# Kernel optimization log

Measured on AMD Instinct MI355X. Metric: run time of the kernel, lower is better.

## Reference

```python
import jax, jax.numpy as jnp
import numpy as np

N = 50000      # nodes
E = 640000     # edges
DIN = 128      # input feature dim
DOUT = 128     # env net output dim
DACT = 2       # action net output dim (keep/drop logits)
REL = 100      # relation embedding dim (hard-coded in get_net)
T = 2          # num edge types
TAU = 0.5      # gumbel temperature (CoGNN temp)


def _lin(k, i, o):
    return jax.random.normal(k, (o, i), jnp.float32) * np.float32(1.0 / np.sqrt(i))


def _hgn_params(key, din, dout):
    ks = jax.random.split(key, 5)
    return {"W_w": _lin(ks[0], din, dout), "W_b": jnp.zeros((dout,), jnp.float32),
            "Wr_w": _lin(ks[1], REL, dout), "Wr_b": jnp.zeros((dout,), jnp.float32),
            "a_w": _lin(ks[2], 3 * dout, 1), "a_b": jnp.zeros((1,), jnp.float32),
            "Wres_w": _lin(ks[3], din, dout), "Wres_b": jnp.zeros((dout,), jnp.float32),
            "rel_emb": jax.random.normal(ks[4], (T, REL), jnp.float32)}


def setup_inputs():
    key = jax.random.key(0)
    ks = jax.random.split(key, 8)
    inp = {"x": jax.random.normal(ks[0], (N, DIN), jnp.float32),
           "edge_index": jax.random.randint(ks[1], (2, E), 0, N, jnp.int32),
           "edge_type": jax.random.randint(ks[2], (E,), 0, T, jnp.int32)}
    u_in = jax.random.uniform(ks[3], (N, DACT), jnp.float32, 1e-6, 1.0 - 1e-6)
    u_out = jax.random.uniform(ks[4], (N, DACT), jnp.float32, 1e-6, 1.0 - 1e-6)
    inp["g_in"] = -jnp.log(-jnp.log(u_in))    # Gumbel(0,1) noise
    inp["g_out"] = -jnp.log(-jnp.log(u_out))
    for name, k, dout in (("inA", ks[5], DACT), ("outA", ks[6], DACT), ("env", ks[7], DOUT)):
        for pk, pv in _hgn_params(k, DIN, dout).items():
            inp[name + "_" + pk] = pv
    return inp


def _simple_hgn(x, src, dst, etype, W_w, W_b, Wr_w, Wr_b, a_w, a_b, Wres_w, Wres_b, rel_emb, mask=None):
    # out = scatter_add_dst( alpha_e * W x_src ) + W_res x   (SimpleHGN, add aggr)
    n = x.shape[0]
    dout = W_w.shape[0]
    h = x @ W_w.T + W_b                       # [N, dout] = W(x)
    r = rel_emb @ Wr_w.T + Wr_b               # [T, dout] = W_r(rel_emb)
    # a(cat(W(x_i), W(x_j), W_r(rel))) decomposed into three per-node/per-type dot products
    a1, a2, a3 = a_w[0, :dout], a_w[0, dout:2 * dout], a_w[0, 2 * dout:]
    s_dst = h @ a1                            # [N]
    s_src = h @ a2                            # [N]
    s_rel = r @ a3                            # [T]
    logits = jax.nn.leaky_relu(s_dst[dst] + s_src[src] + s_rel[etype] + a_b[0], 0.2)  # [E]
    if mask is not None:
        logits = jnp.where(mask, logits, -1e9)
    m = jax.ops.segment_max(logits, dst, num_segments=n)
    e = jnp.exp(logits - m[dst])
    if mask is not None:
        e = jnp.where(mask, e, 0.0)
    denom = jax.ops.segment_sum(e, dst, num_segments=n)
    alpha = e / jnp.maximum(denom[dst], 1e-16)   # edge softmax over incoming edges of each target
    aggr = jax.ops.segment_sum(h[src] * alpha[:, None], dst, num_segments=n)
    return aggr + x @ Wres_w.T + Wres_b


def _gumbel_hard(logits, g):
    y = jax.nn.softmax((logits + g) / TAU, axis=-1)
    y_hard = jax.nn.one_hot(jnp.argmax(y, axis=-1), y.shape[-1], dtype=y.dtype)
    return y_hard + y - jax.lax.stop_gradient(y)   # straight-through (hard=True)


def reference(x, edge_index, edge_type, g_in, g_out,
              inA_W_w, inA_W_b, inA_Wr_w, inA_Wr_b, inA_a_w, inA_a_b, inA_Wres_w, inA_Wres_b, inA_rel_emb,
              outA_W_w, outA_W_b, outA_Wr_w, outA_Wr_b, outA_a_w, outA_a_b, outA_Wres_w, outA_Wres_b, outA_rel_emb,
              env_W_w, env_W_b, env_Wr_w, env_Wr_b, env_a_w, env_a_b, env_Wres_w, env_Wres_b, env_rel_emb):
    src, dst = edge_index[0], edge_index[1]
    in_logits = _simple_hgn(x, src, dst, edge_type, inA_W_w, inA_W_b, inA_Wr_w, inA_Wr_b,
                            inA_a_w, inA_a_b, inA_Wres_w, inA_Wres_b, inA_rel_emb)
    out_logits = _simple_hgn(x, src, dst, edge_type, outA_W_w, outA_W_b, outA_Wr_w, outA_Wr_b,
                             outA_a_w, outA_a_b, outA_Wres_w, outA_Wres_b, outA_rel_emb)
    in_p = _gumbel_hard(in_logits, g_in)
    out_p = _gumbel_hard(out_logits, g_out)
    edge_weight = in_p[:, 0][dst] * out_p[:, 0][src]   # keep_in[v] * keep_out[u]
    mask = edge_weight > 0                              # hard edge filtering, non-differentiable as in torch
    return _simple_hgn(x, src, dst, edge_type, env_W_w, env_W_b, env_Wr_w, env_Wr_b,
                       env_a_w, env_a_b, env_Wres_w, env_Wres_b, env_rel_emb, mask=mask)
```

## Files before the change

### kernel.cpp

```cpp
#include <hip/hip_runtime.h>
#include <hip/hip_bf16.h>
#include <hip/hip_fp16.h>
#include <cstddef>

#define N_NODES 50000
#define N_EDGES 640000
#define DEG_CAP 48

__device__ __forceinline__ float lrelu(float z) { return z >= 0.f ? z : 0.2f * z; }

__device__ __forceinline__ unsigned short f2bf(float f) {
    unsigned u = __builtin_bit_cast(unsigned, f);
    u += 0x7FFFu + ((u >> 16) & 1u);
    return (unsigned short)(u >> 16);
}
__device__ __forceinline__ float bf2f(unsigned short h) {
    unsigned u = ((unsigned)h) << 16;
    return __builtin_bit_cast(float, u);
}

typedef __attribute__((ext_vector_type(8))) short short8;
typedef __attribute__((ext_vector_type(4))) float floatx4;

__global__ __launch_bounds__(256) void k_setup(
    const float* __restrict__ x,
    const float* __restrict__ rel_in, const float* __restrict__ Wr_in,
    const float* __restrict__ Wrb_in,
    const float* __restrict__ rel_out, const float* __restrict__ Wr_out,
    const float* __restrict__ Wrb_out,
    const float* __restrict__ rel_env, const float* __restrict__ Wr_env,
    const float* __restrict__ Wrb_env,
    const float* __restrict__ Wi, const float* __restrict__ Wib,
    const float* __restrict__ WiR, const float* __restrict__ WiRb,
    const float* __restrict__ ai,
    const float* __restrict__ Wo, const float* __restrict__ Wob,
    const float* __restrict__ WoR, const float* __restrict__ WoRb,
    const float* __restrict__ ao,
    const float* __restrict__ eW, const float* __restrict__ eWb,
    const float* __restrict__ eWR, const float* __restrict__ ea,
    float* __restrict__ srel,
    unsigned short* __restrict__ wh, unsigned short* __restrict__ wl,
    float4* __restrict__ dstT, float4* __restrict__ srcPack,
    float4* __restrict__ res_pack)
{
    int b = blockIdx.x;
    int tid = threadIdx.x;

    if (b == 0) {
        __shared__ float red[256];
        __shared__ float rs[8];
        {
            int tt = tid >> 7, j = tid & 127;
            float acc = 0.f;
            for (int k = 0; k < 100; ++k) acc += rel_env[tt * 100 + k] * Wr_env[j * 100 + k];
            acc += Wrb_env[j];
            red[tid] = acc * ea[256 + j];
        }
        if (tid < 8) {
            int net = tid >> 2, tt = (tid >> 1) & 1, j = tid & 1;
            const float* re = net ? rel_out : rel_in;
            const float* wr = net ? Wr_out : Wr_in;
            const float* wb = net ? Wrb_out : Wrb_in;
            float acc = 0.f;
            for (int k = 0; k < 100; ++k) acc += re[tt * 100 + k] * wr[j * 100 + k];
            rs[tid] = acc + wb[j];
        }
        __syncthreads();
        if (tid < 2) {
            float s = 0.f;
            for (int j = 0; j < 128; ++j) s += red[tid * 128 + j];
            srel[4 + tid] = s;
        } else if (tid == 2) {
            srel[0] = rs[0] * ai[4] + rs[1] * ai[5];
            srel[1] = rs[2] * ai[4] + rs[3] * ai[5];
        } else if (tid == 3) {
            srel[2] = rs[4] * ao[4] + rs[5] * ao[5];
            srel[3] = rs[6] * ao[4] + rs[7] * ao[5];
        }
        return;
    }
    if (b < 129) {
        int i = (b - 1) * 256 + tid;
        float v = (i < 16384) ? eW[i] : eWR[i - 16384];
        unsigned short h = f2bf(v);
        wh[i] = h;
        wl[i] = f2bf(v - bf2f(h));
        return;
    }

    __shared__ float sw[10][128];
    __shared__ float vb[2];
    {
        int row = tid >> 5, c4 = tid & 31;
        const float* src;
        switch (row) {
            case 0: src = Wi;        break;
            case 1: src = Wi + 128;  break;
            case 2: src = WiR;       break;
            case 3: src = WiR + 128; break;
            case 4: src = Wo;        break;
            case 5: src = Wo + 128;  break;
            case 6: src = WoR;       break;
            default: src = WoR + 128; break;
        }
        float4 v = ((const float4*)src)[c4];
        sw[row][c4 * 4 + 0] = v.x; sw[row][c4 * 4 + 1] = v.y;
        sw[row][c4 * 4 + 2] = v.z; sw[row][c4 * 4 + 3] = v.w;
    }
    {
        int half = tid >> 7, k = tid & 127;
        const float* av = ea + half * 128;
        float s = 0.f;
        for (int j = 0; j < 128; ++j) s += eW[j * 128 + k] * av[j];
        sw[8 + half][k] = s;
    }
    if (tid < 2) {
        const float* av2 = ea + tid * 128;
        float sb = 0.f;
        for (int j = 0; j < 128; ++j) sb += eWb[j] * av2[j];
        vb[tid] = sb;
    }
    __syncthreads();
    int n = (b - 129) * 256 + tid;
    if (n >= N_NODES) return;
    const float4* xr = (const float4*)(x + (size_t)n * 128);
    float a0 = 0, a1 = 0, a2 = 0, a3 = 0, a4 = 0, a5 = 0, a6 = 0, a7 = 0;
    float a8 = 0, a9 = 0;
#pragma unroll 8
    for (int k4 = 0; k4 < 32; ++k4) {
        float4 v = xr[k4];
        int k = k4 * 4;
        a0 += v.x * sw[0][k] + v.y * sw[0][k + 1] + v.z * sw[0][k + 2] + v.w * sw[0][k + 3];
        a1 += v.x * sw[1][k] + v.y * sw[1][k + 1] + v.z * sw[1][k + 2] + v.w * sw[1][k + 3];
        a2 += v.x * sw[2][k] + v.y * sw[2][k + 1] + v.z * sw[2][k + 2] + v.w * sw[2][k + 3];
        a3 += v.x * sw[3][k] + v.y * sw[3][k + 1] + v.z * sw[3][k + 2] + v.w * sw[3][k + 3];
        a4 += v.x * sw[4][k] + v.y * sw[4][k + 1] + v.z * sw[4][k + 2] + v.w * sw[4][k + 3];
        a5 += v.x * sw[5][k] + v.y * sw[5][k + 1] + v.z * sw[5][k + 2] + v.w * sw[5][k + 3];
        a6 += v.x * sw[6][k] + v.y * sw[6][k + 1] + v.z * sw[6][k + 2] + v.w * sw[6][k + 3];
        a7 += v.x * sw[7][k] + v.y * sw[7][k + 1] + v.z * sw[7][k + 2] + v.w * sw[7][k + 3];
        a8 += v.x * sw[8][k] + v.y * sw[8][k + 1] + v.z * sw[8][k + 2] + v.w * sw[8][k + 3];
        a9 += v.x * sw[9][k] + v.y * sw[9][k + 1] + v.z * sw[9][k + 2] + v.w * sw[9][k + 3];
    }
    float hi0 = a0 + Wib[0], hi1 = a1 + Wib[1];
    float ri0 = a2 + WiRb[0], ri1 = a3 + WiRb[1];
    float ho0 = a4 + Wob[0], ho1 = a5 + Wob[1];
    float ro0 = a6 + WoRb[0], ro1 = a7 + WoRb[1];
    float sdi = hi0 * ai[0] + hi1 * ai[1];
    float ssi = hi0 * ai[2] + hi1 * ai[3];
    float sdo = ho0 * ao[0] + ho1 * ao[1];
    float sso = ho0 * ao[2] + ho1 * ao[3];
    dstT[n]           = make_float4(sdi, sdo, a8 + vb[0], 0.f);
    srcPack[2 * n]     = make_float4(ssi, sso, a9 + vb[1], 0.f);
    srcPack[2 * n + 1] = make_float4(hi0, hi1, ho0, ho1);
    res_pack[n]       = make_float4(ri0, ri1, ro0, ro1);
}

__global__ __launch_bounds__(256) void k_scatter(
    const int* __restrict__ ei, const int* __restrict__ et,
    const float4* __restrict__ dstT, const float4* __restrict__ srcPack,
    const float* __restrict__ srel, const float* __restrict__ ab_env,
    int* __restrict__ cursor, unsigned long long* __restrict__ recs)
{
    int e = blockIdx.x * 256 + threadIdx.x;
    if (e >= N_EDGES) return;
    int src = ei[e], dst = ei[N_EDGES + e], t = et[e];
    float s4 = srel[4], s5 = srel[5];
    float abe = ab_env[0];
    float4 dT = dstT[dst];
    float4 sT = srcPack[2 * src];
    float le = lrelu(dT.z + sT.z + (t ? s5 : s4) + abe);
    int pos = atomicAdd(&cursor[dst], 1);
    if (pos < DEG_CAP) {
        unsigned lo = (unsigned)(src | (t << 20));
        unsigned hi = (unsigned)__float_as_int(__expf(le));
        unsigned long long rec = ((unsigned long long)hi << 32) | lo;
        __builtin_nontemporal_store(rec, &recs[dst * DEG_CAP + pos]);
    }
}

__global__ __launch_bounds__(256) void k_action_seg(
    const int* __restrict__ cursor, const unsigned long long* __restrict__ recs,
    const float4* __restrict__ dstT, const float4* __restrict__ srcPack,
    const float4* __restrict__ res_pack,
    const float* __restrict__ srel,
    const float* __restrict__ ab_in, const float* __restrict__ ab_out,
    const float* __restrict__ g_in, const float* __restrict__ g_out,
    unsigned char* __restrict__ flags)
{
    int gid = blockIdx.x * 256 + threadIdx.x;
    int n = gid >> 2, sub = gid & 3;
    if (n >= N_NODES) return;
    int cnt = min(cursor[n], DEG_CAP);
    int st = n * DEG_CAP;
    float s0 = srel[0], s1 = srel[1], s2 = srel[2], s3 = srel[3];
    float abi = ab_in[0], abo = ab_out[0];
    float4 dT = dstT[n];
    float ni0 = 0, ni1 = 0, di = 0, no0 = 0, no1 = 0, dob = 0;
    for (int i = sub; i < cnt; i += 4) {
        unsigned long long rec = recs[st + i];
        int src = (int)(rec & 0xFFFFFu);
        int t = (int)((rec >> 20) & 0xFFFu);
        float4 sT = srcPack[2 * src];
        float4 hp = srcPack[2 * src + 1];
        float li = lrelu(dT.x + sT.x + (t ? s1 : s0) + abi);
        float lo = lrelu(dT.y + sT.y + (t ? s3 : s2) + abo);
        float ein = __expf(li), eout = __expf(lo);
        di  += ein;  ni0 += ein * hp.x;  ni1 += ein * hp.y;
        dob += eout; no0 += eout * hp.z; no1 += eout * hp.w;
    }
#pragma unroll
    for (int o = 1; o < 4; o <<= 1) {
        ni0 += __shfl_down(ni0, o); ni1 += __shfl_down(ni1, o);
        di  += __shfl_down(di,  o);
        no0 += __shfl_down(no0, o); no1 += __shfl_down(no1, o);
        dob += __shfl_down(dob, o);
    }
    if (sub == 0) {
        float4 rp = res_pack[n];
        float dinv = 1.f / fmaxf(di, 1e-16f);
        float l0 = ni0 * dinv + rp.x;
        float l1 = ni1 * dinv + rp.y;
        float2 gi = ((const float2*)g_in)[n];
        int in0 = (l0 + gi.x) >= (l1 + gi.y);
        float oinv = 1.f / fmaxf(dob, 1e-16f);
        float m0 = no0 * oinv + rp.z;
        float m1 = no1 * oinv + rp.w;
        float2 go = ((const float2*)g_out)[n];
        int out0 = (m0 + go.x) >= (m1 + go.y);
        flags[n] = (unsigned char)(in0 | (out0 << 1));
    }
}

__global__ __launch_bounds__(256, 2) void k_env_mfma(
    const float* __restrict__ x,
    const unsigned short* __restrict__ wh, const unsigned short* __restrict__ wl,
    const float* __restrict__ Wb, const float* __restrict__ WRb,
    __half* __restrict__ h_env, float* __restrict__ dout)
{
    int tid = threadIdx.x;
    int lane = tid & 63;
    int wv = tid >> 6;
    int l15 = lane & 15;
    int quad = lane >> 4;
    int jbase = wv * 64;

    short8 bh[4][4], bl[4][4];
    float bias[4];
#pragma unroll
    for (int jtl = 0; jtl < 4; ++jtl) {
        int j = jbase + jtl * 16 + l15;
        bias[jtl] = (j < 128) ? Wb[j] : WRb[j - 128];
#pragma unroll
        for (int ks = 0; ks < 4; ++ks) {
            size_t o = (size_t)j * 128 + ks * 32 + quad * 8;
            bh[jtl][ks] = *(const short8*)(wh + o);
            bl[jtl][ks] = *(const short8*)(wl + o);
        }
    }

    for (int t = blockIdx.x; t < 3125; t += gridDim.x) {
        int node = t * 16 + l15;
        const float4* ap = (const float4*)(x + (size_t)node * 128 + quad * 8);
        float4 f[8];
#pragma unroll
        for (int ks = 0; ks < 4; ++ks) {
            f[2 * ks]     = ap[ks * 8];
            f[2 * ks + 1] = ap[ks * 8 + 1];
        }
        short8 ah[4], al[4];
#pragma unroll
        for (int ks = 0; ks < 4; ++ks) {
            float av[8] = {f[2 * ks].x, f[2 * ks].y, f[2 * ks].z, f[2 * ks].w,
                           f[2 * ks + 1].x, f[2 * ks + 1].y, f[2 * ks + 1].z, f[2 * ks + 1].w};
#pragma unroll
            for (int i = 0; i < 8; ++i) {
                unsigned short h = f2bf(av[i]);
                ah[ks][i] = (short)h;
                al[ks][i] = (short)f2bf(av[i] - bf2f(h));
            }
        }
        floatx4 acc[4];
#pragma unroll
        for (int jtl = 0; jtl < 4; ++jtl) acc[jtl] = (floatx4)(0.f);
#pragma unroll
        for (int ks = 0; ks < 4; ++ks) {
#pragma unroll
            for (int jtl = 0; jtl < 4; ++jtl) {
                acc[jtl] = __builtin_amdgcn_mfma_f32_16x16x32_bf16(ah[ks], bh[jtl][ks], acc[jtl], 0, 0, 0);
                acc[jtl] = __builtin_amdgcn_mfma_f32_16x16x32_bf16(al[ks], bh[jtl][ks], acc[jtl], 0, 0, 0);
                acc[jtl] = __builtin_amdgcn_mfma_f32_16x16x32_bf16(ah[ks], bl[jtl][ks], acc[jtl], 0, 0, 0);
            }
        }
        int nb = t * 16 + quad * 4;
        if (wv < 2) {
#pragma unroll
            for (int jtl = 0; jtl < 4; ++jtl) {
                int j = jbase + jtl * 16 + l15;
#pragma unroll
                for (int r = 0; r < 4; ++r)
                    h_env[(size_t)(nb + r) * 128 + j] = __float2half(acc[jtl][r] + bias[jtl]);
            }
        } else {
#pragma unroll
            for (int jtl = 0; jtl < 4; ++jtl) {
                int j = jbase - 128 + jtl * 16 + l15;
#pragma unroll
                for (int r = 0; r < 4; ++r)
                    dout[(size_t)(nb + r) * 128 + j] = acc[jtl][r] + bias[jtl];
            }
        }
    }
}

__global__ __launch_bounds__(256) void k_aggr(
    const int* __restrict__ cursor,
    const unsigned long long* __restrict__ recs, const unsigned char* __restrict__ flags,
    const __half* __restrict__ h_env, float* __restrict__ dout)
{
    __shared__ int   s_src[4][64];
    __shared__ float s_w[4][64];
    int tid = threadIdx.x;
    int lane = tid & 63;
    int wv = tid >> 6;
    int n = blockIdx.x * 4 + wv;
    if (n >= N_NODES) return;
    if (!(flags[n] & 1)) return;
    int cnt = min(cursor[n], DEG_CAP);
    int st = n * DEG_CAP;
    float ax = 0.f, ay = 0.f, den = 0.f;
    const __half2* h2 = (const __half2*)h_env;
    {
        int i = lane;
        bool act = false; int src = 0; float wgt = 0.f;
        if (i < cnt) {
            unsigned long long rec = recs[st + i];
            src = (int)(rec & 0xFFFFFu);
            wgt = __int_as_float((int)(rec >> 32));
            act = (flags[src] & 2) != 0;
        }
        unsigned long long bal = __ballot(act);
        int m = __popcll(bal);
        if (act) {
            int pos = __popcll(bal & ((1ull << lane) - 1));
            s_src[wv][pos] = src;
            s_w[wv][pos] = wgt;
        }
        __builtin_amdgcn_wave_barrier();
        int k = 0;
        for (; k + 4 <= m; k += 4) {
            int s0 = s_src[wv][k], s1 = s_src[wv][k + 1];
            int s2 = s_src[wv][k + 2], s3 = s_src[wv][k + 3];
            float w0 = s_w[wv][k], w1 = s_w[wv][k + 1];
            float w2 = s_w[wv][k + 2], w3 = s_w[wv][k + 3];
            float2 f0 = __half22float2(h2[(size_t)s0 * 64 + lane]);
            float2 f1 = __half22float2(h2[(size_t)s1 * 64 + lane]);
            float2 f2 = __half22float2(h2[(size_t)s2 * 64 + lane]);
            float2 f3 = __half22float2(h2[(size_t)s3 * 64 + lane]);
            den += (w0 + w1) + (w2 + w3);
            ax += w0 * f0.x + w1 * f1.x + w2 * f2.x + w3 * f3.x;
            ay += w0 * f0.y + w1 * f1.y + w2 * f2.y + w3 * f3.y;
        }
        for (; k < m; ++k) {
            int s0 = s_src[wv][k];
            float w0 = s_w[wv][k];
            float2 f0 = __half22float2(h2[(size_t)s0 * 64 + lane]);
            den += w0; ax += w0 * f0.x; ay += w0 * f0.y;
        }
    }
    float inv = 1.f / fmaxf(den, 1e-16f);
    float2* op = (float2*)dout + (size_t)n * 64 + lane;
    float2 r = *op;
    r.x = ax * inv + r.x;
    r.y = ay * inv + r.y;
    *op = r;
}

extern "C" void kernel_launch(void* const* d_in, const int* in_sizes, int n_in,
                              void* d_out, int out_size, void* d_ws, size_t ws_size,
                              hipStream_t stream)
{
    const float* x     = (const float*)d_in[0];
    const int*   ei    = (const int*)d_in[1];
    const int*   et    = (const int*)d_in[2];
    const float* g_in  = (const float*)d_in[3];
    const float* g_out = (const float*)d_in[4];
    const float* iW   = (const float*)d_in[5];
    const float* iWb  = (const float*)d_in[6];
    const float* iWr  = (const float*)d_in[7];
    const float* iWrb = (const float*)d_in[8];
    const float* ia   = (const float*)d_in[9];
    const float* iab  = (const float*)d_in[10];
    const float* iWR  = (const float*)d_in[11];
    const float* iWRb = (const float*)d_in[12];
    const float* irel = (const float*)d_in[13];
    const float* oW   = (const float*)d_in[14];
    const float* oWb  = (const float*)d_in[15];
    const float* oWr  = (const float*)d_in[16];
    const float* oWrb = (const float*)d_in[17];
    const float* oa   = (const float*)d_in[18];
    const float* oab  = (const float*)d_in[19];
    const float* oWR  = (const float*)d_in[20];
    const float* oWRb = (const float*)d_in[21];
    const float* orel = (const float*)d_in[22];
    const float* eW   = (const float*)d_in[23];
    const float* eWb  = (const float*)d_in[24];
    const float* eWr  = (const float*)d_in[25];
    const float* eWrb = (const float*)d_in[26];
    const float* ea   = (const float*)d_in[27];
    const float* eab  = (const float*)d_in[28];
    const float* eWR  = (const float*)d_in[29];
    const float* eWRb = (const float*)d_in[30];
    const float* erel = (const float*)d_in[31];
    float* dout = (float*)d_out;

    char* w = (char*)d_ws;
    size_t off = 0;
    auto alloc = [&](size_t bytes) -> char* {
        char* p = w + off;
        off += (bytes + 255) & ~(size_t)255;
        return p;
    };
    int*   cursor  = (int*)alloc((size_t)N_NODES * 4);
    size_t zeroBytes = off;
    float* srel    = (float*)alloc(16 * 4);
    float4* dstT     = (float4*)alloc((size_t)4 * N_NODES * 4);
    float4* srcPack  = (float4*)alloc((size_t)8 * N_NODES * 4);
    float4* res_pack = (float4*)alloc((size_t)4 * N_NODES * 4);
    unsigned char* flags = (unsigned char*)alloc(N_NODES);
    unsigned short* wh = (unsigned short*)alloc((size_t)32768 * 2);
    unsigned short* wl = (unsigned short*)alloc((size_t)32768 * 2);
    unsigned long long* recs = (unsigned long long*)alloc((size_t)N_NODES * DEG_CAP * 8);
    __half* h_env    = (__half*)alloc((size_t)N_NODES * 128 * 2);

    (void)hipMemsetAsync(w, 0, zeroBytes, stream);
    k_setup<<<325, 256, 0, stream>>>(x,
                                     irel, iWr, iWrb, orel, oWr, oWrb, erel, eWr, eWrb,
                                     iW, iWb, iWR, iWRb, ia, oW, oWb, oWR, oWRb, oa,
                                     eW, eWb, eWR, ea,
                                     srel, wh, wl, dstT, srcPack, res_pack);
    k_scatter<<<2500, 256, 0, stream>>>(ei, et, dstT, srcPack, srel, eab,
                                        cursor, recs);
    k_env_mfma<<<512, 256, 0, stream>>>(x, wh, wl, eWb, eWRb, h_env, dout);
    k_action_seg<<<782, 256, 0, stream>>>(cursor, recs, dstT, srcPack, res_pack,
                                          srel, iab, oab, g_in, g_out, flags);
    k_aggr<<<12500, 256, 0, stream>>>(cursor, recs, flags, h_env, dout);
}
```

Before: 246.8 us.

## Precompute action-net edge exponentials in scatter and fold cursor zeroing into setup

The scatter kernel now computes the in/out action attention exponentials per edge alongside the env weight and stores them in a 16-byte record, so the action segment kernel no longer gathers srcPack[2*src] and recomputes lrelu/exp. The separate memset of the cursor array is removed and the zeroing moves into k_setup, which saves one launch. In exchange the record buffer doubles in size, so scatter writes and the record reads in k_aggr move twice the bytes. k_aggr now reads 16-byte records even though it only needs 8 bytes of each.

```diff
diff --git a/kernel.cpp b/kernel.cpp
--- a/kernel.cpp
+++ b/kernel.cpp
@@ -21,6 +21,7 @@
 
 typedef __attribute__((ext_vector_type(8))) short short8;
 typedef __attribute__((ext_vector_type(4))) float floatx4;
+typedef __attribute__((ext_vector_type(4))) int intx4;
 
 __global__ __launch_bounds__(256) void k_setup(
     const float* __restrict__ x,
@@ -41,7 +42,7 @@
     float* __restrict__ srel,
     unsigned short* __restrict__ wh, unsigned short* __restrict__ wl,
     float4* __restrict__ dstT, float4* __restrict__ srcPack,
-    float4* __restrict__ res_pack)
+    float4* __restrict__ res_pack, int* __restrict__ cursor)
 {
     int b = blockIdx.x;
     int tid = threadIdx.x;
@@ -87,6 +88,9 @@
         wl[i] = f2bf(v - bf2f(h));
         return;
     }
+
+    int n = (b - 129) * 256 + tid;
+    if (n < N_NODES) cursor[n] = 0;
 
     __shared__ float sw[10][128];
     __shared__ float vb[2];
@@ -121,7 +125,6 @@
         vb[tid] = sb;
     }
     __syncthreads();
-    int n = (b - 129) * 256 + tid;
     if (n >= N_NODES) return;
     const float4* xr = (const float4*)(x + (size_t)n * 128);
     float a0 = 0, a1 = 0, a2 = 0, a3 = 0, a4 = 0, a5 = 0, a6 = 0, a7 = 0;
@@ -158,32 +161,36 @@
 __global__ __launch_bounds__(256) void k_scatter(
     const int* __restrict__ ei, const int* __restrict__ et,
     const float4* __restrict__ dstT, const float4* __restrict__ srcPack,
-    const float* __restrict__ srel, const float* __restrict__ ab_env,
-    int* __restrict__ cursor, unsigned long long* __restrict__ recs)
+    const float* __restrict__ srel,
+    const float* __restrict__ ab_in, const float* __restrict__ ab_out,
+    const float* __restrict__ ab_env,
+    int* __restrict__ cursor, intx4* __restrict__ recs)
 {
     int e = blockIdx.x * 256 + threadIdx.x;
     if (e >= N_EDGES) return;
     int src = ei[e], dst = ei[N_EDGES + e], t = et[e];
-    float s4 = srel[4], s5 = srel[5];
-    float abe = ab_env[0];
+    float s0 = srel[0], s1 = srel[1], s2 = srel[2];
+    float s3 = srel[3], s4 = srel[4], s5 = srel[5];
+    float abi = ab_in[0], abo = ab_out[0], abe = ab_env[0];
     float4 dT = dstT[dst];
     float4 sT = srcPack[2 * src];
+    float li = lrelu(dT.x + sT.x + (t ? s1 : s0) + abi);
+    float lo = lrelu(dT.y + sT.y + (t ? s3 : s2) + abo);
     float le = lrelu(dT.z + sT.z + (t ? s5 : s4) + abe);
     int pos = atomicAdd(&cursor[dst], 1);
     if (pos < DEG_CAP) {
-        unsigned lo = (unsigned)(src | (t << 20));
-        unsigned hi = (unsigned)__float_as_int(__expf(le));
-        unsigned long long rec = ((unsigned long long)hi << 32) | lo;
+        intx4 rec;
+        rec[0] = src | (t << 20);
+        rec[1] = __float_as_int(__expf(le));
+        rec[2] = __float_as_int(__expf(li));
+        rec[3] = __float_as_int(__expf(lo));
         __builtin_nontemporal_store(rec, &recs[dst * DEG_CAP + pos]);
     }
 }
 
 __global__ __launch_bounds__(256) void k_action_seg(
-    const int* __restrict__ cursor, const unsigned long long* __restrict__ recs,
-    const float4* __restrict__ dstT, const float4* __restrict__ srcPack,
-    const float4* __restrict__ res_pack,
-    const float* __restrict__ srel,
-    const float* __restrict__ ab_in, const float* __restrict__ ab_out,
+    const int* __restrict__ cursor, const intx4* __restrict__ recs,
+    const float4* __restrict__ srcPack, const float4* __restrict__ res_pack,
     const float* __restrict__ g_in, const float* __restrict__ g_out,
     unsigned char* __restrict__ flags)
 {
@@ -192,19 +199,12 @@
     if (n >= N_NODES) return;
     int cnt = min(cursor[n], DEG_CAP);
     int st = n * DEG_CAP;
-    float s0 = srel[0], s1 = srel[1], s2 = srel[2], s3 = srel[3];
-    float abi = ab_in[0], abo = ab_out[0];
-    float4 dT = dstT[n];
     float ni0 = 0, ni1 = 0, di = 0, no0 = 0, no1 = 0, dob = 0;
     for (int i = sub; i < cnt; i += 4) {
-        unsigned long long rec = recs[st + i];
-        int src = (int)(rec & 0xFFFFFu);
-        int t = (int)((rec >> 20) & 0xFFFu);
-        float4 sT = srcPack[2 * src];
+        intx4 r = recs[st + i];
+        int src = r[0] & 0xFFFFF;
         float4 hp = srcPack[2 * src + 1];
-        float li = lrelu(dT.x + sT.x + (t ? s1 : s0) + abi);
-        float lo = lrelu(dT.y + sT.y + (t ? s3 : s2) + abo);
-        float ein = __expf(li), eout = __expf(lo);
+        float ein = __int_as_float(r[2]), eout = __int_as_float(r[3]);
         di  += ein;  ni0 += ein * hp.x;  ni1 += ein * hp.y;
         dob += eout; no0 += eout * hp.z; no1 += eout * hp.w;
     }
@@ -314,7 +314,7 @@
 
 __global__ __launch_bounds__(256) void k_aggr(
     const int* __restrict__ cursor,
-    const unsigned long long* __restrict__ recs, const unsigned char* __restrict__ flags,
+    const intx4* __restrict__ recs, const unsigned char* __restrict__ flags,
     const __half* __restrict__ h_env, float* __restrict__ dout)
 {
     __shared__ int   s_src[4][64];
@@ -333,9 +333,9 @@
         int i = lane;
         bool act = false; int src = 0; float wgt = 0.f;
         if (i < cnt) {
-            unsigned long long rec = recs[st + i];
-            src = (int)(rec & 0xFFFFFu);
-            wgt = __int_as_float((int)(rec >> 32));
+            intx4 r = recs[st + i];
+            src = r[0] & 0xFFFFF;
+            wgt = __int_as_float(r[1]);
             act = (flags[src] & 2) != 0;
         }
         unsigned long long bal = __ballot(act);
@@ -421,7 +421,6 @@
         return p;
     };
     int*   cursor  = (int*)alloc((size_t)N_NODES * 4);
-    size_t zeroBytes = off;
     float* srel    = (float*)alloc(16 * 4);
     float4* dstT     = (float4*)alloc((size_t)4 * N_NODES * 4);
     float4* srcPack  = (float4*)alloc((size_t)8 * N_NODES * 4);
@@ -429,19 +428,18 @@
     unsigned char* flags = (unsigned char*)alloc(N_NODES);
     unsigned short* wh = (unsigned short*)alloc((size_t)32768 * 2);
     unsigned short* wl = (unsigned short*)alloc((size_t)32768 * 2);
-    unsigned long long* recs = (unsigned long long*)alloc((size_t)N_NODES * DEG_CAP * 8);
+    intx4* recs      = (intx4*)alloc((size_t)N_NODES * DEG_CAP * 16);
     __half* h_env    = (__half*)alloc((size_t)N_NODES * 128 * 2);
 
-    (void)hipMemsetAsync(w, 0, zeroBytes, stream);
     k_setup<<<325, 256, 0, stream>>>(x,
                                      irel, iWr, iWrb, orel, oWr, oWrb, erel, eWr, eWrb,
                                      iW, iWb, iWR, iWRb, ia, oW, oWb, oWR, oWRb, oa,
                                      eW, eWb, eWR, ea,
-                                     srel, wh, wl, dstT, srcPack, res_pack);
-    k_scatter<<<2500, 256, 0, stream>>>(ei, et, dstT, srcPack, srel, eab,
-                                        cursor, recs);
+                                     srel, wh, wl, dstT, srcPack, res_pack, cursor);
+    k_scatter<<<2500, 256, 0, stream>>>(ei, et, dstT, srcPack, srel,
+                                        iab, oab, eab, cursor, recs);
     k_env_mfma<<<512, 256, 0, stream>>>(x, wh, wl, eWb, eWRb, h_env, dout);
-    k_action_seg<<<782, 256, 0, stream>>>(cursor, recs, dstT, srcPack, res_pack,
-                                          srel, iab, oab, g_in, g_out, flags);
+    k_action_seg<<<782, 256, 0, stream>>>(cursor, recs, srcPack, res_pack,
+                                          g_in, g_out, flags);
     k_aggr<<<12500, 256, 0, stream>>>(cursor, recs, flags, h_env, dout);
 }
```

Measured after the change: 252.8 us. 1.02x slower.

## Fuse edge scatter and env MFMA GEMM into one kernel, drop memset

Applied to the files above, without the earlier changes.

Merges the edge-scatter kernel and the env-net MFMA GEMM into a single launch. Blocks 0-511 run the GEMM and the remaining 625 blocks each bucket 4 edges per thread, so the two independent stages can overlap on the GPU. The cursor array is now zeroed inside k_setup rather than by a separate memset, and the scatter stores become plain stores instead of nontemporal ones. This removes a launch and a memset, in exchange for mixed-role blocks that may compete for CUs and registers.

```diff
diff --git a/kernel.cpp b/kernel.cpp
--- a/kernel.cpp
+++ b/kernel.cpp
@@ -41,7 +41,7 @@
     float* __restrict__ srel,
     unsigned short* __restrict__ wh, unsigned short* __restrict__ wl,
     float4* __restrict__ dstT, float4* __restrict__ srcPack,
-    float4* __restrict__ res_pack)
+    float4* __restrict__ res_pack, int* __restrict__ cursor)
 {
     int b = blockIdx.x;
     int tid = threadIdx.x;
@@ -87,6 +87,9 @@
         wl[i] = f2bf(v - bf2f(h));
         return;
     }
+
+    int n = (b - 129) * 256 + tid;
+    if (n < N_NODES) cursor[n] = 0;
 
     __shared__ float sw[10][128];
     __shared__ float vb[2];
@@ -121,7 +124,6 @@
         vb[tid] = sb;
     }
     __syncthreads();
-    int n = (b - 129) * 256 + tid;
     if (n >= N_NODES) return;
     const float4* xr = (const float4*)(x + (size_t)n * 128);
     float a0 = 0, a1 = 0, a2 = 0, a3 = 0, a4 = 0, a5 = 0, a6 = 0, a7 = 0;
@@ -155,26 +157,121 @@
     res_pack[n]       = make_float4(ri0, ri1, ro0, ro1);
 }
 
-__global__ __launch_bounds__(256) void k_scatter(
+__global__ __launch_bounds__(256, 2) void k_mid(
+    const float* __restrict__ x,
+    const unsigned short* __restrict__ wh, const unsigned short* __restrict__ wl,
+    const float* __restrict__ Wb, const float* __restrict__ WRb,
+    __half* __restrict__ h_env, float* __restrict__ dout,
     const int* __restrict__ ei, const int* __restrict__ et,
     const float4* __restrict__ dstT, const float4* __restrict__ srcPack,
     const float* __restrict__ srel, const float* __restrict__ ab_env,
     int* __restrict__ cursor, unsigned long long* __restrict__ recs)
 {
-    int e = blockIdx.x * 256 + threadIdx.x;
-    if (e >= N_EDGES) return;
-    int src = ei[e], dst = ei[N_EDGES + e], t = et[e];
-    float s4 = srel[4], s5 = srel[5];
-    float abe = ab_env[0];
-    float4 dT = dstT[dst];
-    float4 sT = srcPack[2 * src];
-    float le = lrelu(dT.z + sT.z + (t ? s5 : s4) + abe);
-    int pos = atomicAdd(&cursor[dst], 1);
-    if (pos < DEG_CAP) {
-        unsigned lo = (unsigned)(src | (t << 20));
-        unsigned hi = (unsigned)__float_as_int(__expf(le));
-        unsigned long long rec = ((unsigned long long)hi << 32) | lo;
-        __builtin_nontemporal_store(rec, &recs[dst * DEG_CAP + pos]);
+    int b = blockIdx.x;
+    int tid = threadIdx.x;
+
+    if (b >= 512) {
+        int base = (b - 512) * 1024 + tid;
+        float s4 = srel[4], s5 = srel[5];
+        float abe = ab_env[0];
+        int src[4], dst[4], t[4];
+#pragma unroll
+        for (int k = 0; k < 4; ++k) {
+            int e = base + k * 256;
+            src[k] = ei[e];
+            dst[k] = ei[N_EDGES + e];
+            t[k]   = et[e];
+        }
+        float4 dT[4], sT[4];
+#pragma unroll
+        for (int k = 0; k < 4; ++k) {
+            dT[k] = dstT[dst[k]];
+            sT[k] = srcPack[2 * src[k]];
+        }
+#pragma unroll
+        for (int k = 0; k < 4; ++k) {
+            float le = lrelu(dT[k].z + sT[k].z + (t[k] ? s5 : s4) + abe);
+            int pos = atomicAdd(&cursor[dst[k]], 1);
+            if (pos < DEG_CAP) {
+                unsigned lo = (unsigned)(src[k] | (t[k] << 20));
+                unsigned hi = (unsigned)__float_as_int(__expf(le));
+                recs[dst[k] * DEG_CAP + pos] = ((unsigned long long)hi << 32) | lo;
+            }
+        }
+        return;
+    }
+
+    int lane = tid & 63;
+    int wv = tid >> 6;
+    int l15 = lane & 15;
+    int quad = lane >> 4;
+    int jbase = wv * 64;
+
+    short8 bh[4][4], bl[4][4];
+    float bias[4];
+#pragma unroll
+    for (int jtl = 0; jtl < 4; ++jtl) {
+        int j = jbase + jtl * 16 + l15;
+        bias[jtl] = (j < 128) ? Wb[j] : WRb[j - 128];
+#pragma unroll
+        for (int ks = 0; ks < 4; ++ks) {
+            size_t o = (size_t)j * 128 + ks * 32 + quad * 8;
+            bh[jtl][ks] = *(const short8*)(wh + o);
+            bl[jtl][ks] = *(const short8*)(wl + o);
+        }
+    }
+
+    for (int t = b; t < 3125; t += 512) {
+        int node = t * 16 + l15;
+        const float4* ap = (const float4*)(x + (size_t)node * 128 + quad * 8);
+        float4 f[8];
+#pragma unroll
+        for (int ks = 0; ks < 4; ++ks) {
+            f[2 * ks]     = ap[ks * 8];
+            f[2 * ks + 1] = ap[ks * 8 + 1];
+        }
+        short8 ah[4], al[4];
+#pragma unroll
+        for (int ks = 0; ks < 4; ++ks) {
+            float av[8] = {f[2 * ks].x, f[2 * ks].y, f[2 * ks].z, f[2 * ks].w,
+                           f[2 * ks + 1].x, f[2 * ks + 1].y, f[2 * ks + 1].z, f[2 * ks + 1].w};
+#pragma unroll
+            for (int i = 0; i < 8; ++i) {
+                unsigned short h = f2bf(av[i]);
+                ah[ks][i] = (short)h;
+                al[ks][i] = (short)f2bf(av[i] - bf2f(h));
+            }
+        }
+        floatx4 acc[4];
+#pragma unroll
+        for (int jtl = 0; jtl < 4; ++jtl) acc[jtl] = (floatx4)(0.f);
+#pragma unroll
+        for (int ks = 0; ks < 4; ++ks) {
+#pragma unroll
+            for (int jtl = 0; jtl < 4; ++jtl) {
+                acc[jtl] = __builtin_amdgcn_mfma_f32_16x16x32_bf16(ah[ks], bh[jtl][ks], acc[jtl], 0, 0, 0);
+                acc[jtl] = __builtin_amdgcn_mfma_f32_16x16x32_bf16(al[ks], bh[jtl][ks], acc[jtl], 0, 0, 0);
+                acc[jtl] = __builtin_amdgcn_mfma_f32_16x16x32_bf16(ah[ks], bl[jtl][ks], acc[jtl], 0, 0, 0);
+            }
+        }
+        int nb = t * 16 + quad * 4;
+        if (wv < 2) {
+#pragma unroll
+            for (int jtl = 0; jtl < 4; ++jtl) {
+                int j = jbase + jtl * 16 + l15;
+#pragma unroll
+                for (int r = 0; r < 4; ++r)
+                    h_env[(size_t)(nb + r) * 128 + j] = __float2half(acc[jtl][r] + bias[jtl]);
+            }
+        } else {
+#pragma unroll
+            for (int jtl = 0; jtl < 4; ++jtl) {
+                int j = jbase - 128 + jtl * 16 + l15;
+#pragma unroll
+                for (int r = 0; r < 4; ++r)
+                    dout[(size_t)(nb + r) * 128 + j] = acc[jtl][r] + bias[jtl];
+            }
+        }
     }
 }
 
@@ -228,87 +325,6 @@
         float2 go = ((const float2*)g_out)[n];
         int out0 = (m0 + go.x) >= (m1 + go.y);
         flags[n] = (unsigned char)(in0 | (out0 << 1));
-    }
-}
-
-__global__ __launch_bounds__(256, 2) void k_env_mfma(
-    const float* __restrict__ x,
-    const unsigned short* __restrict__ wh, const unsigned short* __restrict__ wl,
-    const float* __restrict__ Wb, const float* __restrict__ WRb,
-    __half* __restrict__ h_env, float* __restrict__ dout)
-{
-    int tid = threadIdx.x;
-    int lane = tid & 63;
-    int wv = tid >> 6;
-    int l15 = lane & 15;
-    int quad = lane >> 4;
-    int jbase = wv * 64;
-
-    short8 bh[4][4], bl[4][4];
-    float bias[4];
-#pragma unroll
-    for (int jtl = 0; jtl < 4; ++jtl) {
-        int j = jbase + jtl * 16 + l15;
-        bias[jtl] = (j < 128) ? Wb[j] : WRb[j - 128];
-#pragma unroll
-        for (int ks = 0; ks < 4; ++ks) {
-            size_t o = (size_t)j * 128 + ks * 32 + quad * 8;
-            bh[jtl][ks] = *(const short8*)(wh + o);
-            bl[jtl][ks] = *(const short8*)(wl + o);
-        }
-    }
-
-    for (int t = blockIdx.x; t < 3125; t += gridDim.x) {
-        int node = t * 16 + l15;
-        const float4* ap = (const float4*)(x + (size_t)node * 128 + quad * 8);
-        float4 f[8];
-#pragma unroll
-        for (int ks = 0; ks < 4; ++ks) {
-            f[2 * ks]     = ap[ks * 8];
-            f[2 * ks + 1] = ap[ks * 8 + 1];
-        }
-        short8 ah[4], al[4];
-#pragma unroll
-        for (int ks = 0; ks < 4; ++ks) {
-            float av[8] = {f[2 * ks].x, f[2 * ks].y, f[2 * ks].z, f[2 * ks].w,
-                           f[2 * ks + 1].x, f[2 * ks + 1].y, f[2 * ks + 1].z, f[2 * ks + 1].w};
-#pragma unroll
-            for (int i = 0; i < 8; ++i) {
-                unsigned short h = f2bf(av[i]);
-                ah[ks][i] = (short)h;
-                al[ks][i] = (short)f2bf(av[i] - bf2f(h));
-            }
-        }
-        floatx4 acc[4];
-#pragma unroll
-        for (int jtl = 0; jtl < 4; ++jtl) acc[jtl] = (floatx4)(0.f);
-#pragma unroll
-        for (int ks = 0; ks < 4; ++ks) {
-#pragma unroll
-            for (int jtl = 0; jtl < 4; ++jtl) {
-                acc[jtl] = __builtin_amdgcn_mfma_f32_16x16x32_bf16(ah[ks], bh[jtl][ks], acc[jtl], 0, 0, 0);
-                acc[jtl] = __builtin_amdgcn_mfma_f32_16x16x32_bf16(al[ks], bh[jtl][ks], acc[jtl], 0, 0, 0);
-                acc[jtl] = __builtin_amdgcn_mfma_f32_16x16x32_bf16(ah[ks], bl[jtl][ks], acc[jtl], 0, 0, 0);
-            }
-        }
-        int nb = t * 16 + quad * 4;
-        if (wv < 2) {
-#pragma unroll
-            for (int jtl = 0; jtl < 4; ++jtl) {
-                int j = jbase + jtl * 16 + l15;
-#pragma unroll
-                for (int r = 0; r < 4; ++r)
-                    h_env[(size_t)(nb + r) * 128 + j] = __float2half(acc[jtl][r] + bias[jtl]);
-            }
-        } else {
-#pragma unroll
-            for (int jtl = 0; jtl < 4; ++jtl) {
-                int j = jbase - 128 + jtl * 16 + l15;
-#pragma unroll
-                for (int r = 0; r < 4; ++r)
-                    dout[(size_t)(nb + r) * 128 + j] = acc[jtl][r] + bias[jtl];
-            }
-        }
     }
 }
 
@@ -421,7 +437,6 @@
         return p;
     };
     int*   cursor  = (int*)alloc((size_t)N_NODES * 4);
-    size_t zeroBytes = off;
     float* srel    = (float*)alloc(16 * 4);
     float4* dstT     = (float4*)alloc((size_t)4 * N_NODES * 4);
     float4* srcPack  = (float4*)alloc((size_t)8 * N_NODES * 4);
@@ -432,15 +447,13 @@
     unsigned long long* recs = (unsigned long long*)alloc((size_t)N_NODES * DEG_CAP * 8);
     __half* h_env    = (__half*)alloc((size_t)N_NODES * 128 * 2);
 
-    (void)hipMemsetAsync(w, 0, zeroBytes, stream);
     k_setup<<<325, 256, 0, stream>>>(x,
                                      irel, iWr, iWrb, orel, oWr, oWrb, erel, eWr, eWrb,
                                      iW, iWb, iWR, iWRb, ia, oW, oWb, oWR, oWRb, oa,
                                      eW, eWb, eWR, ea,
-                                     srel, wh, wl, dstT, srcPack, res_pack);
-    k_scatter<<<2500, 256, 0, stream>>>(ei, et, dstT, srcPack, srel, eab,
-                                        cursor, recs);
-    k_env_mfma<<<512, 256, 0, stream>>>(x, wh, wl, eWb, eWRb, h_env, dout);
+                                     srel, wh, wl, dstT, srcPack, res_pack, cursor);
+    k_mid<<<1137, 256, 0, stream>>>(x, wh, wl, eWb, eWRb, h_env, dout,
+                                    ei, et, dstT, srcPack, srel, eab, cursor, recs);
     k_action_seg<<<782, 256, 0, stream>>>(cursor, recs, dstT, srcPack, res_pack,
                                           srel, iab, oab, g_in, g_out, flags);
     k_aggr<<<12500, 256, 0, stream>>>(cursor, recs, flags, h_env, dout);
```

Measured after the change: 233.7 us. 5.3% less time.
